# Kernel tuning notes

Measured on AMD Instinct MI355X. Metric: run time of the kernel, lower is better.

Reference implementation:

```python
import jax, jax.numpy as jnp
import numpy as np

T_IN, B, H = 12, 65536, 64
T_OUT = 12
OVERLAP = 3


def setup_inputs() -> dict:
    key = jax.random.key(0)
    ks = jax.random.split(key, 9)
    return {
        "encoder_out": jax.random.normal(ks[0], (T_IN, B, H), dtype=jnp.float32),
        "encoder_hid": jax.random.normal(ks[1], (B, H), dtype=jnp.float32),
        "last": jax.random.normal(ks[2], (B, OVERLAP), dtype=jnp.float32),
        # GRUCell params (PyTorch layout: weight_ih (3H, in), weight_hh (3H, H), gate order r,z,n)
        "W_ih": jax.random.normal(ks[3], (3 * H, OVERLAP), dtype=jnp.float32) * 0.1,
        "W_hh": jax.random.normal(ks[4], (3 * H, H), dtype=jnp.float32) * 0.1,
        "b_ih": jax.random.normal(ks[5], (3 * H,), dtype=jnp.float32) * 0.1,
        "b_hh": jax.random.normal(ks[6], (3 * H,), dtype=jnp.float32) * 0.1,
        # Linear hidden -> 1
        "W_lin": jax.random.normal(ks[7], (1, H), dtype=jnp.float32) * 0.1,
        "b_lin": jax.random.normal(ks[8], (1,), dtype=jnp.float32) * 0.1,
    }


def _gru_cell(x, h, W_ih, W_hh, b_ih, b_hh):
    gi = x @ W_ih.T + b_ih  # (B, 3H)
    gh = h @ W_hh.T + b_hh  # (B, 3H)
    i_r, i_z, i_n = jnp.split(gi, 3, axis=-1)
    h_r, h_z, h_n = jnp.split(gh, 3, axis=-1)
    r = jax.nn.sigmoid(i_r + h_r)
    z = jax.nn.sigmoid(i_z + h_z)
    n = jnp.tanh(i_n + r * h_n)
    return (1.0 - z) * n + z * h


def reference(encoder_out, encoder_hid, last, W_ih, W_hh, b_ih, b_hh, W_lin, b_lin):
    def step(carry, _):
        hidden, lst = carry
        # attention over encoder time steps (softmax along time axis 0)
        attn_w = jnp.einsum('tbk,bk->tb', encoder_out, hidden)
        attn_w = jax.nn.softmax(attn_w, axis=0)
        context = jnp.einsum('tbk,tb->bk', encoder_out, attn_w)
        hidden = hidden + context
        hidden = _gru_cell(lst, hidden, W_ih, W_hh, b_ih, b_hh)
        out = hidden @ W_lin.T + b_lin  # (B, 1)
        # torch uses out.detach() when feeding back
        lst = jnp.concatenate([jax.lax.stop_gradient(out), lst[:, :OVERLAP - 1]], axis=-1)
        return (hidden, lst), out

    (_, _), outs = jax.lax.scan(step, (encoder_hid, last), None, length=T_OUT)
    # outs: (T_OUT, B, 1) -> (B, T_OUT), matching torch.cat(decoder_out, dim=-1)
    return jnp.transpose(outs[:, :, 0], (1, 0))
```

## Files before the change

kernel.cpp:

```cpp
#include <hip/hip_runtime.h>


#define TT 12
#define BB 65536
#define HH 64

typedef _Float16 half8 __attribute__((ext_vector_type(8)));
typedef _Float16 half4 __attribute__((ext_vector_type(4)));
typedef float    f32x4 __attribute__((ext_vector_type(4)));
typedef float    f32x2 __attribute__((ext_vector_type(2)));

#define L2E 1.44269504088896f

__device__ __forceinline__ float ex2(float x){ return __builtin_amdgcn_exp2f(x); }
__device__ __forceinline__ float sigm(float x){ return 1.0f/(1.0f + ex2(-L2E*x)); }
__device__ __forceinline__ float tanh_(float x){ return 1.0f - 2.0f/(ex2(2.0f*L2E*x)+1.0f); }

template<int N>
__device__ __forceinline__ float ror_add(float x){
    int s = __builtin_amdgcn_update_dpp(0, __float_as_int(x), 0x120+N, 0xF, 0xF, false);
    return x + __int_as_float(s);
}
__device__ __forceinline__ float sum16(float x){
    x = ror_add<1>(x); x = ror_add<2>(x); x = ror_add<4>(x); x = ror_add<8>(x);
    return x;
}

__global__ __launch_bounds__(256, 2)
void decoder_kernel(const float* __restrict__ enc,
                    const float* __restrict__ hid0,
                    const float* __restrict__ last0,
                    const float* __restrict__ Wih,
                    const float* __restrict__ Whh,
                    const float* __restrict__ bih,
                    const float* __restrict__ bhh,
                    const float* __restrict__ Wlin,
                    const float* __restrict__ blin,
                    float* __restrict__ out)
{
    __shared__ __align__(16) _Float16 sHi[16*72];
    __shared__ __align__(16) _Float16 sLo[16*72];
    __shared__ __align__(16) float    sGh[16*196];

    const int tid  = threadIdx.x;
    const int wv   = tid >> 6;
    const int lane = tid & 63;
    const int q    = lane & 15;
    const int quad = lane >> 4;
    const int m    = wv*4 + quad;
    const size_t b = (size_t)blockIdx.x*16 + m;

    f32x4 e4[TT];
    #pragma unroll
    for (int t=0;t<TT;++t)
        e4[t] = *(const f32x4*)(enc + ((size_t)t*BB + b)*HH + 4*q);

    f32x4 h = *(const f32x4*)(hid0 + b*HH + 4*q);
    float l0 = last0[b*3+0], l1 = last0[b*3+1], l2 = last0[b*3+2];
    float bl = blin[0];

    f32x4 wr0,wr1,wr2, wz0,wz1,wz2, wn0,wn1,wn2;
    {
        #pragma unroll
        for (int j=0;j<4;++j){
            int r0 = (0*64 + 4*q + j)*3, r1 = (1*64 + 4*q + j)*3, r2 = (2*64 + 4*q + j)*3;
            wr0[j]=Wih[r0+0]; wr1[j]=Wih[r0+1]; wr2[j]=Wih[r0+2];
            wz0[j]=Wih[r1+0]; wz1[j]=Wih[r1+1]; wz2[j]=Wih[r1+2];
            wn0[j]=Wih[r2+0]; wn1[j]=Wih[r2+1]; wn2[j]=Wih[r2+2];
        }
    }
    f32x4 bc0, bc1, bi2, bh2;
    #pragma unroll
    for (int j=0;j<4;++j){
        bc0[j] = bih[      4*q+j] + bhh[      4*q+j];
        bc1[j] = bih[ 64 + 4*q+j] + bhh[ 64 + 4*q+j];
        bi2[j] = bih[128 + 4*q+j];
        bh2[j] = bhh[128 + 4*q+j];
    }
    f32x4 wl = *(const f32x4*)(Wlin + 4*q);

    half8 wfhi[3][2], wflo[3][2];
    #pragma unroll
    for (int c=0;c<3;++c){
        int jout = (wv*3+c)*16 + q;
        #pragma unroll
        for (int kc=0;kc<2;++kc){
            const float* src = Whh + jout*64 + kc*32 + quad*8;
            half8 vh, vl;
            #pragma unroll
            for (int jj=0;jj<8;++jj){
                float w = src[jj];
                _Float16 whi = (_Float16)w;
                vh[jj] = whi;
                vl[jj] = (_Float16)(w - (float)whi);
            }
            wfhi[c][kc] = vh;
            wflo[c][kc] = vl;
        }
    }

    for (int s=0;s<TT;++s){
        float a[TT];
        #pragma unroll
        for (int t=0;t<TT;++t){
            f32x2 p2 = e4[t].xy * h.xy;
            p2 += e4[t].zw * h.zw;
            a[t] = sum16(p2.x + p2.y);
        }
        float mx01 = fmaxf(a[0],a[1]), mx23 = fmaxf(a[2],a[3]), mx45 = fmaxf(a[4],a[5]);
        float mx67 = fmaxf(a[6],a[7]), mx89 = fmaxf(a[8],a[9]), mxab = fmaxf(a[10],a[11]);
        float mx = fmaxf(fmaxf(fmaxf(mx01,mx23),fmaxf(mx45,mx67)),fmaxf(mx89,mxab));
        float nm = -mx*L2E;
        #pragma unroll
        for (int t=0;t<TT;++t) a[t] = ex2(__builtin_fmaf(a[t], L2E, nm));
        float s01=a[0]+a[1], s23=a[2]+a[3], s45=a[4]+a[5], s67=a[6]+a[7], s89=a[8]+a[9], sab=a[10]+a[11];
        float ss = ((s01+s23)+(s45+s67)) + (s89+sab);
        float inv = 1.0f/ss;
        f32x4 ctxA = {0.f,0.f,0.f,0.f}, ctxB = {0.f,0.f,0.f,0.f};
        #pragma unroll
        for (int t=0;t<TT;t+=2){
            ctxA += e4[t]   * (f32x4)(a[t]);
            ctxB += e4[t+1] * (f32x4)(a[t+1]);
        }
        h += (ctxA + ctxB) * (f32x4)(inv);

        half4 hhi, hlo;
        #pragma unroll
        for (int j=0;j<4;++j){
            _Float16 hh = (_Float16)h[j];
            hhi[j] = hh;
            hlo[j] = (_Float16)(h[j] - (float)hh);
        }
        *(half4*)&sHi[m*72 + 4*q] = hhi;
        *(half4*)&sLo[m*72 + 4*q] = hlo;
        __syncthreads();

        half8 ahi0 = *(half8*)&sHi[q*72 +  0 + quad*8];
        half8 ahi1 = *(half8*)&sHi[q*72 + 32 + quad*8];
        half8 alo0 = *(half8*)&sLo[q*72 +  0 + quad*8];
        half8 alo1 = *(half8*)&sLo[q*72 + 32 + quad*8];
        #pragma unroll
        for (int c=0;c<3;++c){
            f32x4 acc = {0.f,0.f,0.f,0.f};
            acc = __builtin_amdgcn_mfma_f32_16x16x32_f16(ahi0, wfhi[c][0], acc, 0,0,0);
            acc = __builtin_amdgcn_mfma_f32_16x16x32_f16(ahi1, wfhi[c][1], acc, 0,0,0);
            acc = __builtin_amdgcn_mfma_f32_16x16x32_f16(ahi0, wflo[c][0], acc, 0,0,0);
            acc = __builtin_amdgcn_mfma_f32_16x16x32_f16(ahi1, wflo[c][1], acc, 0,0,0);
            acc = __builtin_amdgcn_mfma_f32_16x16x32_f16(alo0, wfhi[c][0], acc, 0,0,0);
            acc = __builtin_amdgcn_mfma_f32_16x16x32_f16(alo1, wfhi[c][1], acc, 0,0,0);
            int jcol = (wv*3+c)*16 + q;
            #pragma unroll
            for (int r=0;r<4;++r)
                sGh[(quad*4+r)*196 + jcol] = acc[r];
        }
        __syncthreads();

        f32x4 ghr = *(f32x4*)&sGh[m*196 +   0 + 4*q];
        f32x4 ghz = *(f32x4*)&sGh[m*196 +  64 + 4*q];
        f32x4 ghn = *(f32x4*)&sGh[m*196 + 128 + 4*q];

        f32x4 gr4 = bc0 + ghr;  gr4 += wr0*(f32x4)(l0); gr4 += wr1*(f32x4)(l1); gr4 += wr2*(f32x4)(l2);
        f32x4 gz4 = bc1 + ghz;  gz4 += wz0*(f32x4)(l0); gz4 += wz1*(f32x4)(l1); gz4 += wz2*(f32x4)(l2);
        f32x4 gn4 = bi2;        gn4 += wn0*(f32x4)(l0); gn4 += wn1*(f32x4)(l1); gn4 += wn2*(f32x4)(l2);
        f32x4 hb  = ghn + bh2;

        float o = 0.f;
        #pragma unroll
        for (int j=0;j<4;++j){
            float r = sigm(gr4[j]);
            float z = sigm(gz4[j]);
            float n = tanh_(gn4[j] + r*hb[j]);
            float hn = (1.f - z)*n + z*h[j];
            h[j] = hn;
            o += hn * wl[j];
        }
        o = sum16(o) + bl;
        if (q == 0) out[b*TT + s] = o;
        l2 = l1; l1 = l0; l0 = o;
    }
}

extern "C" void kernel_launch(void* const* d_in, const int* in_sizes, int n_in,
                              void* d_out, int out_size, void* d_ws, size_t ws_size,
                              hipStream_t stream)
{
    const float* enc  = (const float*)d_in[0];
    const float* hid0 = (const float*)d_in[1];
    const float* lst  = (const float*)d_in[2];
    const float* Wih  = (const float*)d_in[3];
    const float* Whh  = (const float*)d_in[4];
    const float* bih  = (const float*)d_in[5];
    const float* bhh  = (const float*)d_in[6];
    const float* Wlin = (const float*)d_in[7];
    const float* blin = (const float*)d_in[8];
    decoder_kernel<<<BB/16, 256, 0, stream>>>(enc, hid0, lst, Wih, Whh, bih, bhh,
                                              Wlin, blin, (float*)d_out);
}
```

Measured before the change: 442.3 us.

## Fold GRU input projection and biases into MFMA via augmented K columns

Appends the three feedback inputs and a constant one to the hidden-state tile as extra K columns, so the W_ih projection and biases are computed on the matrix cores instead of per-lane FMAs. Each wave now owns one 16-column slice of every gate (r, z, n_h, n_i) rather than three gate-major column blocks. This adds a fourth output block and extra MFMAs, and stores W_ih and biases in fp16 (the hi/lo split covers the inputs but not those weights), which may cost accuracy. The softmax max reduction also switches to three-input max.

```diff
diff --git a/kernel.cpp b/kernel.cpp
--- a/kernel.cpp
+++ b/kernel.cpp
@@ -25,6 +25,12 @@
     x = ror_add<1>(x); x = ror_add<2>(x); x = ror_add<4>(x); x = ror_add<8>(x);
     return x;
 }
+
+__device__ __forceinline__ float max3f(float a, float b, float c){
+    return fmaxf(fmaxf(a,b),c);
+}
+
+#define MFMA16(A,B,C) __builtin_amdgcn_mfma_f32_16x16x32_f16(A,B,C,0,0,0)
 
 __global__ __launch_bounds__(256, 2)
 void decoder_kernel(const float* __restrict__ enc,
@@ -38,9 +44,9 @@
                     const float* __restrict__ blin,
                     float* __restrict__ out)
 {
-    __shared__ __align__(16) _Float16 sHi[16*72];
-    __shared__ __align__(16) _Float16 sLo[16*72];
-    __shared__ __align__(16) float    sGh[16*196];
+    __shared__ __align__(16) _Float16 sHi[16*96];
+    __shared__ __align__(16) _Float16 sLo[16*96];
+    __shared__ __align__(16) float    sGh[16*260];
 
     const int tid  = threadIdx.x;
     const int wv   = tid >> 6;
@@ -49,6 +55,11 @@
     const int quad = lane >> 4;
     const int m    = wv*4 + quad;
     const size_t b = (size_t)blockIdx.x*16 + m;
+    const int jq   = wv*16 + q;
+
+    for (int i = tid; i < 16*96; i += 256){
+        if ((i % 96) >= 68){ sHi[i] = (_Float16)0; sLo[i] = (_Float16)0; }
+    }
 
     f32x4 e4[TT];
     #pragma unroll
@@ -58,45 +69,44 @@
     f32x4 h = *(const f32x4*)(hid0 + b*HH + 4*q);
     float l0 = last0[b*3+0], l1 = last0[b*3+1], l2 = last0[b*3+2];
     float bl = blin[0];
-
-    f32x4 wr0,wr1,wr2, wz0,wz1,wz2, wn0,wn1,wn2;
+    f32x4 wl = *(const f32x4*)(Wlin + 4*q);
+
+    half8 bR0h,bR0l,bR1h,bR1l, bZ0h,bZ0l,bZ1h,bZ1l, bN0h,bN0l,bN1h,bN1l;
     {
         #pragma unroll
-        for (int j=0;j<4;++j){
-            int r0 = (0*64 + 4*q + j)*3, r1 = (1*64 + 4*q + j)*3, r2 = (2*64 + 4*q + j)*3;
-            wr0[j]=Wih[r0+0]; wr1[j]=Wih[r0+1]; wr2[j]=Wih[r0+2];
-            wz0[j]=Wih[r1+0]; wz1[j]=Wih[r1+1]; wz2[j]=Wih[r1+2];
-            wn0[j]=Wih[r2+0]; wn1[j]=Wih[r2+1]; wn2[j]=Wih[r2+2];
-        }
-    }
-    f32x4 bc0, bc1, bi2, bh2;
+        for (int g=0; g<3; ++g){
+            int row = g*64 + jq;
+            #pragma unroll
+            for (int kc=0; kc<2; ++kc){
+                const float* src = Whh + row*64 + kc*32 + quad*8;
+                half8 vh, vl;
+                #pragma unroll
+                for (int jj=0;jj<8;++jj){
+                    float w = src[jj];
+                    _Float16 whi = (_Float16)w;
+                    vh[jj] = whi;
+                    vl[jj] = (_Float16)(w - (float)whi);
+                }
+                if (g==0){ if(kc==0){bR0h=vh;bR0l=vl;} else {bR1h=vh;bR1l=vl;} }
+                else if (g==1){ if(kc==0){bZ0h=vh;bZ0l=vl;} else {bZ1h=vh;bZ1l=vl;} }
+                else { if(kc==0){bN0h=vh;bN0l=vl;} else {bN1h=vh;bN1l=vl;} }
+            }
+        }
+    }
+    half8 bR2h, bZ2h, bN2h, bI2h;
     #pragma unroll
-    for (int j=0;j<4;++j){
-        bc0[j] = bih[      4*q+j] + bhh[      4*q+j];
-        bc1[j] = bih[ 64 + 4*q+j] + bhh[ 64 + 4*q+j];
-        bi2[j] = bih[128 + 4*q+j];
-        bh2[j] = bhh[128 + 4*q+j];
-    }
-    f32x4 wl = *(const f32x4*)(Wlin + 4*q);
-
-    half8 wfhi[3][2], wflo[3][2];
-    #pragma unroll
-    for (int c=0;c<3;++c){
-        int jout = (wv*3+c)*16 + q;
-        #pragma unroll
-        for (int kc=0;kc<2;++kc){
-            const float* src = Whh + jout*64 + kc*32 + quad*8;
-            half8 vh, vl;
-            #pragma unroll
-            for (int jj=0;jj<8;++jj){
-                float w = src[jj];
-                _Float16 whi = (_Float16)w;
-                vh[jj] = whi;
-                vl[jj] = (_Float16)(w - (float)whi);
-            }
-            wfhi[c][kc] = vh;
-            wflo[c][kc] = vl;
-        }
+    for (int jj=0;jj<8;++jj){ bR2h[jj]=(_Float16)0; bZ2h[jj]=(_Float16)0; bN2h[jj]=(_Float16)0; bI2h[jj]=(_Float16)0; }
+    if (quad == 0){
+        #pragma unroll
+        for (int jj=0;jj<3;++jj){
+            bR2h[jj] = (_Float16)Wih[(      jq)*3 + jj];
+            bZ2h[jj] = (_Float16)Wih[( 64 + jq)*3 + jj];
+            bI2h[jj] = (_Float16)Wih[(128 + jq)*3 + jj];
+        }
+        bR2h[3] = (_Float16)(bih[      jq] + bhh[      jq]);
+        bZ2h[3] = (_Float16)(bih[ 64 + jq] + bhh[ 64 + jq]);
+        bN2h[3] = (_Float16)(bhh[128 + jq]);
+        bI2h[3] = (_Float16)(bih[128 + jq]);
     }
 
     for (int s=0;s<TT;++s){
@@ -107,9 +117,9 @@
             p2 += e4[t].zw * h.zw;
             a[t] = sum16(p2.x + p2.y);
         }
-        float mx01 = fmaxf(a[0],a[1]), mx23 = fmaxf(a[2],a[3]), mx45 = fmaxf(a[4],a[5]);
-        float mx67 = fmaxf(a[6],a[7]), mx89 = fmaxf(a[8],a[9]), mxab = fmaxf(a[10],a[11]);
-        float mx = fmaxf(fmaxf(fmaxf(mx01,mx23),fmaxf(mx45,mx67)),fmaxf(mx89,mxab));
+        float m0 = max3f(a[0],a[1],a[2]),  m1 = max3f(a[3],a[4],a[5]);
+        float m2 = max3f(a[6],a[7],a[8]),  m3 = max3f(a[9],a[10],a[11]);
+        float mx = fmaxf(max3f(m0,m1,m2), m3);
         float nm = -mx*L2E;
         #pragma unroll
         for (int t=0;t<TT;++t) a[t] = ex2(__builtin_fmaf(a[t], L2E, nm));
@@ -131,45 +141,71 @@
             hhi[j] = hh;
             hlo[j] = (_Float16)(h[j] - (float)hh);
         }
-        *(half4*)&sHi[m*72 + 4*q] = hhi;
-        *(half4*)&sLo[m*72 + 4*q] = hlo;
+        *(half4*)&sHi[m*96 + 4*q] = hhi;
+        *(half4*)&sLo[m*96 + 4*q] = hlo;
+        if (q == 0){
+            _Float16 a0=(_Float16)l0, a1=(_Float16)l1, a2=(_Float16)l2;
+            half4 th = {a0, a1, a2, (_Float16)1.0f};
+            half4 tl = {(_Float16)(l0-(float)a0), (_Float16)(l1-(float)a1),
+                        (_Float16)(l2-(float)a2), (_Float16)0.0f};
+            *(half4*)&sHi[m*96 + 64] = th;
+            *(half4*)&sLo[m*96 + 64] = tl;
+        }
         __syncthreads();
 
-        half8 ahi0 = *(half8*)&sHi[q*72 +  0 + quad*8];
-        half8 ahi1 = *(half8*)&sHi[q*72 + 32 + quad*8];
-        half8 alo0 = *(half8*)&sLo[q*72 +  0 + quad*8];
-        half8 alo1 = *(half8*)&sLo[q*72 + 32 + quad*8];
-        #pragma unroll
-        for (int c=0;c<3;++c){
-            f32x4 acc = {0.f,0.f,0.f,0.f};
-            acc = __builtin_amdgcn_mfma_f32_16x16x32_f16(ahi0, wfhi[c][0], acc, 0,0,0);
-            acc = __builtin_amdgcn_mfma_f32_16x16x32_f16(ahi1, wfhi[c][1], acc, 0,0,0);
-            acc = __builtin_amdgcn_mfma_f32_16x16x32_f16(ahi0, wflo[c][0], acc, 0,0,0);
-            acc = __builtin_amdgcn_mfma_f32_16x16x32_f16(ahi1, wflo[c][1], acc, 0,0,0);
-            acc = __builtin_amdgcn_mfma_f32_16x16x32_f16(alo0, wfhi[c][0], acc, 0,0,0);
-            acc = __builtin_amdgcn_mfma_f32_16x16x32_f16(alo1, wfhi[c][1], acc, 0,0,0);
-            int jcol = (wv*3+c)*16 + q;
-            #pragma unroll
-            for (int r=0;r<4;++r)
-                sGh[(quad*4+r)*196 + jcol] = acc[r];
+        half8 ahi0 = *(half8*)&sHi[q*96 +  0 + quad*8];
+        half8 ahi1 = *(half8*)&sHi[q*96 + 32 + quad*8];
+        half8 ahi2 = *(half8*)&sHi[q*96 + 64 + quad*8];
+        half8 alo0 = *(half8*)&sLo[q*96 +  0 + quad*8];
+        half8 alo1 = *(half8*)&sLo[q*96 + 32 + quad*8];
+        half8 alo2 = *(half8*)&sLo[q*96 + 64 + quad*8];
+
+        {
+            f32x4 acc = {0.f,0.f,0.f,0.f};
+            acc = MFMA16(ahi0,bR0h,acc); acc = MFMA16(ahi1,bR1h,acc);
+            acc = MFMA16(ahi0,bR0l,acc); acc = MFMA16(ahi1,bR1l,acc);
+            acc = MFMA16(alo0,bR0h,acc); acc = MFMA16(alo1,bR1h,acc);
+            acc = MFMA16(ahi2,bR2h,acc); acc = MFMA16(alo2,bR2h,acc);
+            #pragma unroll
+            for (int r=0;r<4;++r) sGh[(quad*4+r)*260 +   0 + jq] = acc[r];
+        }
+        {
+            f32x4 acc = {0.f,0.f,0.f,0.f};
+            acc = MFMA16(ahi0,bZ0h,acc); acc = MFMA16(ahi1,bZ1h,acc);
+            acc = MFMA16(ahi0,bZ0l,acc); acc = MFMA16(ahi1,bZ1l,acc);
+            acc = MFMA16(alo0,bZ0h,acc); acc = MFMA16(alo1,bZ1h,acc);
+            acc = MFMA16(ahi2,bZ2h,acc); acc = MFMA16(alo2,bZ2h,acc);
+            #pragma unroll
+            for (int r=0;r<4;++r) sGh[(quad*4+r)*260 +  64 + jq] = acc[r];
+        }
+        {
+            f32x4 acc = {0.f,0.f,0.f,0.f};
+            acc = MFMA16(ahi0,bN0h,acc); acc = MFMA16(ahi1,bN1h,acc);
+            acc = MFMA16(ahi0,bN0l,acc); acc = MFMA16(ahi1,bN1l,acc);
+            acc = MFMA16(alo0,bN0h,acc); acc = MFMA16(alo1,bN1h,acc);
+            acc = MFMA16(ahi2,bN2h,acc);
+            #pragma unroll
+            for (int r=0;r<4;++r) sGh[(quad*4+r)*260 + 128 + jq] = acc[r];
+        }
+        {
+            f32x4 acc = {0.f,0.f,0.f,0.f};
+            acc = MFMA16(ahi2,bI2h,acc); acc = MFMA16(alo2,bI2h,acc);
+            #pragma unroll
+            for (int r=0;r<4;++r) sGh[(quad*4+r)*260 + 192 + jq] = acc[r];
         }
         __syncthreads();
 
-        f32x4 ghr = *(f32x4*)&sGh[m*196 +   0 + 4*q];
-        f32x4 ghz = *(f32x4*)&sGh[m*196 +  64 + 4*q];
-        f32x4 ghn = *(f32x4*)&sGh[m*196 + 128 + 4*q];
-
-        f32x4 gr4 = bc0 + ghr;  gr4 += wr0*(f32x4)(l0); gr4 += wr1*(f32x4)(l1); gr4 += wr2*(f32x4)(l2);
-        f32x4 gz4 = bc1 + ghz;  gz4 += wz0*(f32x4)(l0); gz4 += wz1*(f32x4)(l1); gz4 += wz2*(f32x4)(l2);
-        f32x4 gn4 = bi2;        gn4 += wn0*(f32x4)(l0); gn4 += wn1*(f32x4)(l1); gn4 += wn2*(f32x4)(l2);
-        f32x4 hb  = ghn + bh2;
+        f32x4 gR  = *(f32x4*)&sGh[m*260 +   0 + 4*q];
+        f32x4 gZ  = *(f32x4*)&sGh[m*260 +  64 + 4*q];
+        f32x4 gNH = *(f32x4*)&sGh[m*260 + 128 + 4*q];
+        f32x4 gNI = *(f32x4*)&sGh[m*260 + 192 + 4*q];
 
         float o = 0.f;
         #pragma unroll
         for (int j=0;j<4;++j){
-            float r = sigm(gr4[j]);
-            float z = sigm(gz4[j]);
-            float n = tanh_(gn4[j] + r*hb[j]);
+            float r = sigm(gR[j]);
+            float z = sigm(gZ[j]);
+            float n = tanh_(gNI[j] + r*gNH[j]);
             float hn = (1.f - z)*n + z*h[j];
             h[j] = hn;
             o += hn * wl[j];
```

Result: slower. 455.0 us (+2.9%).
